# Kernel optimization log

Hardware: AMD Instinct MI355X
Metric: run time of the kernel (lower is better)

The kernel has to match this reference:

```python
import jax, jax.numpy as jnp
import numpy as np

B, S1, S2, D, H, FFN = 4, 1024, 1024, 1024, 16, 4096
DK = D // H  # 64
EPS = 1e-5


def layer_norm(x, g, b):
    m = jnp.mean(x, axis=-1, keepdims=True)
    v = jnp.mean((x - m) ** 2, axis=-1, keepdims=True)
    return (x - m) * jax.lax.rsqrt(v + EPS) * g + b


def cross_attention(y, kvn, mask, qw, kw, vw, ow, ob):
    # y: [B,S1,D], kvn: [B,S2,D], mask: [B,S2] int (0 -> masked)
    q = (y @ qw).reshape(B, S1, H, DK)
    k = (kvn @ kw).reshape(B, S2, H, DK)
    v = (kvn @ vw).reshape(B, S2, H, DK)
    attn = jnp.einsum('bqhd,bkhd->bhqk', q, k) / np.sqrt(DK).astype(np.float32)
    attn = jnp.where(mask[:, None, None, :] == 0, jnp.float32(-1e9), attn)
    attn = jax.nn.softmax(attn, axis=-1)
    out = jnp.einsum('bhqk,bkhd->bqhd', attn, v).reshape(B, S1, H * DK)
    return out @ ow + ob


def setup_inputs() -> dict:
    key = jax.random.key(0)
    ks = jax.random.split(key, 16)
    s = 1.0 / np.sqrt(D)
    inp = {
        'x': jax.random.normal(ks[0], (B, S1, D), jnp.float32),
        'kv': jax.random.normal(ks[1], (B, S2, D), jnp.float32),
        'attn_bias': jax.random.randint(ks[2], (B, S2), 0, 2, jnp.int32),
        'ln1_g': jnp.ones((D,), jnp.float32),
        'ln1_b': jnp.zeros((D,), jnp.float32),
        'qw0': jax.random.normal(ks[3], (D, D), jnp.float32) * s,
        'kw0': jax.random.normal(ks[4], (D, D), jnp.float32) * s,
        'vw0': jax.random.normal(ks[5], (D, D), jnp.float32) * s,
        'ow0': jax.random.normal(ks[6], (D, D), jnp.float32) * s,
        'ob0': jnp.zeros((D,), jnp.float32),
        'qw1': jax.random.normal(ks[7], (D, D), jnp.float32) * s,
        'kw1': jax.random.normal(ks[8], (D, D), jnp.float32) * s,
        'vw1': jax.random.normal(ks[9], (D, D), jnp.float32) * s,
        'ow1': jax.random.normal(ks[10], (D, D), jnp.float32) * s,
        'ob1': jnp.zeros((D,), jnp.float32),
        'ln2_g': jnp.ones((D,), jnp.float32),
        'ln2_b': jnp.zeros((D,), jnp.float32),
        'w1': jax.random.normal(ks[11], (D, FFN), jnp.float32) * s,
        'b1': jnp.zeros((FFN,), jnp.float32),
        'w2': jax.random.normal(ks[12], (FFN, D), jnp.float32) * (1.0 / np.sqrt(FFN)),
        'b2': jnp.zeros((D,), jnp.float32),
    }
    return inp


def reference(x, kv, attn_bias, ln1_g, ln1_b, qw0, kw0, vw0, ow0, ob0,
              qw1, kw1, vw1, ow1, ob1, ln2_g, ln2_b, w1, b1, w2, b2):
    y = layer_norm(x, ln1_g, ln1_b)
    kvn = layer_norm(kv, ln1_g, ln1_b)  # same norm module applied to both
    y = cross_attention(y, kvn, attn_bias, qw0, kw0, vw0, ow0, ob0) + y
    y = cross_attention(y, kvn, attn_bias, qw1, kw1, vw1, ow1, ob1) + y
    x = x + y  # dropout rate 0 -> identity
    y = layer_norm(x, ln2_g, ln2_b)
    y = jax.nn.relu(y @ w1 + b1) @ w2 + b2
    x = x + y
    return x
```

## Files before the change

### kernel.cpp

```cpp
#include <hip/hip_runtime.h>
#include <stdint.h>

typedef unsigned short u16;
typedef __bf16 bf16x8 __attribute__((ext_vector_type(8)));
typedef float f32x4 __attribute__((ext_vector_type(4)));

#define LOG2E 1.4426950408889634f

__device__ __forceinline__ float bf2f(u16 a) {
  union { unsigned u; float f; } v; v.u = ((unsigned)a) << 16; return v.f;
}
__device__ __forceinline__ u16 f2bf(float f) {
  union { float f; unsigned u; } v; v.f = f;
  unsigned r = v.u + 0x7fffu + ((v.u >> 16) & 1u);
  return (u16)(r >> 16);
}
__device__ __forceinline__ u16 f2bf_fast(float f) {
  __bf16 h = (__bf16)f;
  union { __bf16 h; u16 u; } v; v.h = h; return v.u;
}
__device__ __forceinline__ void gl_lds16(const void* g, void* l) {
  __builtin_amdgcn_global_load_lds(
      (const __attribute__((address_space(1))) uint32_t*)g,
      (__attribute__((address_space(3))) uint32_t*)l,
      16, 0, 0);
}

__device__ __forceinline__ int swz(int row, int colu16) {
  return row * 64 + (colu16 ^ (((row ^ (row >> 2)) & 7) << 3));
}

template <int BM, int BN, int MODE>
__global__ __launch_bounds__(256) void gemm_bt(
    const u16* __restrict__ A, const u16* __restrict__ Bt,
    u16* Cbf, float* C32,
    const float* __restrict__ bias,
    const u16* resbf, const float* __restrict__ resx,
    int M, int N, int K, const int* __restrict__ rowcnt)
{
  constexpr int MT = BM / 32, NT = BN / 32;
  constexpr int GA = BM / 32, GB = BN / 32;
  __shared__ u16 sA[BM * 64];
  __shared__ u16 sB[BN * 64];
  const int tid  = threadIdx.x;
  const int wave = tid >> 6, lane = tid & 63;
  const int quad = lane >> 4, l16 = lane & 15;
  const int wm = wave >> 1, wn = wave & 1;
  const int nwg = gridDim.x * gridDim.y;
  const int bid = blockIdx.y * gridDim.x + blockIdx.x;
  const int sw  = (bid & 7) * (nwg >> 3) + (bid >> 3);
  const int m0 = (sw / gridDim.x) * BM, n0 = (sw % gridDim.x) * BN;
  if (rowcnt) {
    int lim = (rowcnt[m0 >> 10] + 63) & ~63;
    if ((m0 & 1023) >= lim) return;
  }

  f32x4 acc[MT][NT] = {};

  for (int k0 = 0; k0 < K; k0 += 64) {
    __syncthreads();
#pragma unroll
    for (int i = 0; i < GA; ++i) {
      int cb = i * 256 + wave * 64;
      int c = cb + lane;
      int row = c >> 3;
      int kcs = (c & 7) ^ ((row ^ (row >> 2)) & 7);
      gl_lds16(A + (size_t)(m0 + row) * K + k0 + kcs * 8, &sA[cb * 8]);
    }
#pragma unroll
    for (int i = 0; i < GB; ++i) {
      int cb = i * 256 + wave * 64;
      int c = cb + lane;
      int row = c >> 3;
      int kcs = (c & 7) ^ ((row ^ (row >> 2)) & 7);
      gl_lds16(Bt + (size_t)(n0 + row) * K + k0 + kcs * 8, &sB[cb * 8]);
    }
    __syncthreads();

#pragma unroll
    for (int kk = 0; kk < 2; ++kk) {
      bf16x8 fa[MT], fb[NT];
#pragma unroll
      for (int mt = 0; mt < MT; ++mt)
        fa[mt] = *(const bf16x8*)&sA[swz(wm * (BM / 2) + mt * 16 + l16, kk * 32 + quad * 8)];
#pragma unroll
      for (int nt = 0; nt < NT; ++nt)
        fb[nt] = *(const bf16x8*)&sB[swz(wn * (BN / 2) + nt * 16 + l16, kk * 32 + quad * 8)];
#pragma unroll
      for (int mt = 0; mt < MT; ++mt)
#pragma unroll
        for (int nt = 0; nt < NT; ++nt)
          acc[mt][nt] = __builtin_amdgcn_mfma_f32_16x16x32_bf16(
              fa[mt], fb[nt], acc[mt][nt], 0, 0, 0);
    }
  }

#pragma unroll
  for (int mt = 0; mt < MT; ++mt) {
#pragma unroll
    for (int nt = 0; nt < NT; ++nt) {
#pragma unroll
      for (int r = 0; r < 4; ++r) {
        int row = m0 + wm * (BM / 2) + mt * 16 + quad * 4 + r;
        int col = n0 + wn * (BN / 2) + nt * 16 + l16;
        size_t idx = (size_t)row * N + col;
        float v = acc[mt][nt][r];
        if constexpr (MODE == 0) {
          Cbf[idx] = f2bf(v);
        } else if constexpr (MODE == 1) {
          v += bias[col] + bf2f(resbf[idx]);
          Cbf[idx] = f2bf(v);
        } else if constexpr (MODE == 2) {
          v = fmaxf(v + bias[col], 0.f);
          Cbf[idx] = f2bf(v);
        } else if constexpr (MODE == 3) {
          v += bias[col] + resx[idx] + bf2f(resbf[idx]);
          C32[idx] = v;
        } else {
          C32[idx] = C32[idx] + v;
        }
      }
    }
  }
}

__global__ __launch_bounds__(256) void transpose64(
    const float* __restrict__ in, u16* __restrict__ out, int R, int Cstride)
{
  __shared__ u16 tile[64][72];
  const int r0 = blockIdx.y * 64, c0 = blockIdx.x * 64;
  const int t = threadIdx.x;
  {
    const int lr = t >> 4, lc = (t & 15) * 4;
#pragma unroll
    for (int h = 0; h < 4; ++h) {
      int row = h * 16 + lr;
      float4 vd = *(const float4*)&in[(size_t)(r0 + row) * Cstride + c0 + lc];
      ushort4 ov;
      ov.x = f2bf(vd.x); ov.y = f2bf(vd.y); ov.z = f2bf(vd.z); ov.w = f2bf(vd.w);
      *(ushort4*)&tile[row][lc] = ov;
    }
  }
  __syncthreads();
  {
    const int lr = t >> 3, lv = t & 7;
#pragma unroll
    for (int h = 0; h < 2; ++h) {
      int orow = h * 32 + lr;
      u16 tmp[8];
#pragma unroll
      for (int j = 0; j < 8; ++j) tmp[j] = tile[lv * 8 + j][orow];
      *(uint4*)&out[(size_t)(c0 + orow) * R + r0 + lv * 8] = *(uint4*)tmp;
    }
  }
}

__global__ __launch_bounds__(256) void mask_scan(
    const int* __restrict__ mask, int* __restrict__ sidx, int* __restrict__ nv)
{
  const int b = blockIdx.x, t = threadIdx.x;
  const int wave = t >> 6, lane = t & 63;
  int m[4]; int cnt = 0;
#pragma unroll
  for (int k = 0; k < 4; ++k) { m[k] = (mask[b * 1024 + t * 4 + k] != 0); cnt += m[k]; }
  int sc = cnt;
  for (int sh = 1; sh < 64; sh <<= 1) {
    int u = __shfl_up(sc, sh);
    if (lane >= sh) sc += u;
  }
  __shared__ int wsum[4];
  if (lane == 63) wsum[wave] = sc;
  __syncthreads();
  int woff = 0;
  for (int w = 0; w < wave; ++w) woff += wsum[w];
  int pos = woff + sc - cnt;
#pragma unroll
  for (int k = 0; k < 4; ++k)
    if (m[k]) sidx[b * 1024 + pos++] = t * 4 + k;
  if (t == 255) nv[b] = wsum[0] + wsum[1] + wsum[2] + wsum[3];
}

__global__ __launch_bounds__(256) void gather_kv(
    const u16* __restrict__ src, const int* __restrict__ sidx,
    const int* __restrict__ nv, u16* __restrict__ dst)
{
  const int t = threadIdx.x, wave = t >> 6, lane = t & 63;
  const int row = blockIdx.x * 4 + wave;
  const int b = row >> 10, i = row & 1023;
  const int n = nv[b];
  const int s = sidx[b * 1024 + (i < n ? i : n - 1)];
  const uint4* sp = (const uint4*)&src[((size_t)(b << 10) + s) * 1024];
  uint4* dp = (uint4*)&dst[(size_t)row * 1024];
  dp[lane] = sp[lane];
  dp[lane + 64] = sp[lane + 64];
}

__global__ __launch_bounds__(256) void vtc_kernel(
    const u16* __restrict__ in, const int* __restrict__ nv,
    u16* __restrict__ out)
{
  __shared__ u16 tile[64][72];
  const int st = blockIdx.x, bh = blockIdx.y;
  const int b = bh >> 4, h = bh & 15;
  const int t = threadIdx.x;
  const int lr = t >> 3, lv = t & 7;
  const int n = nv[b];
  const u16* srcb = in + (size_t)b * 1024 * 2048 + 1024 + h * 64;
#pragma unroll
  for (int half = 0; half < 2; ++half) {
    int i = st * 64 + half * 32 + lr;
    int s = i < n ? i : n - 1;
    uint4 vd = *(const uint4*)&srcb[(size_t)s * 2048 + lv * 8];
    *(uint4*)&tile[half * 32 + lr][lv * 8] = vd;
  }
  __syncthreads();
  u16* dst = out + (size_t)bh * 64 * 1024 + st * 64;
#pragma unroll
  for (int half = 0; half < 2; ++half) {
    int orow = half * 32 + lr;
    u16 tmp[8];
#pragma unroll
    for (int j = 0; j < 8; ++j) tmp[j] = tile[lv * 8 + j][orow];
    *(uint4*)&dst[(size_t)orow * 1024 + lv * 8] = *(uint4*)tmp;
  }
}

__global__ __launch_bounds__(256) void ln_kernel(
    const float* __restrict__ x, const float* __restrict__ g,
    const float* __restrict__ b, u16* __restrict__ outbf)
{
  const int row = blockIdx.x, t = threadIdx.x;
  const int wave = t >> 6, lane = t & 63;
  float4 xv = *(const float4*)&x[(size_t)row * 1024 + t * 4];
  float v0 = xv.x, v1 = xv.y, v2 = xv.z, v3 = xv.w;
  float s = v0 + v1 + v2 + v3;
  float s2 = v0 * v0 + v1 * v1 + v2 * v2 + v3 * v3;
  for (int m = 1; m < 64; m <<= 1) { s += __shfl_xor(s, m); s2 += __shfl_xor(s2, m); }
  __shared__ float ps[4], pq[4];
  if (lane == 0) { ps[wave] = s; pq[wave] = s2; }
  __syncthreads();
  s = ps[0] + ps[1] + ps[2] + ps[3];
  s2 = pq[0] + pq[1] + pq[2] + pq[3];
  float mean = s * (1.f / 1024.f);
  float var = s2 * (1.f / 1024.f) - mean * mean;
  float rs = rsqrtf(var + 1e-5f);
  float4 gv = *(const float4*)&g[t * 4];
  float4 bv = *(const float4*)&b[t * 4];
  ushort4 ov;
  ov.x = f2bf((v0 - mean) * rs * gv.x + bv.x);
  ov.y = f2bf((v1 - mean) * rs * gv.y + bv.y);
  ov.z = f2bf((v2 - mean) * rs * gv.z + bv.z);
  ov.w = f2bf((v3 - mean) * rs * gv.w + bv.w);
  *(ushort4*)&outbf[(size_t)row * 1024 + t * 4] = ov;
}

__global__ __launch_bounds__(256) void ln_add_kernel(
    const float* __restrict__ x, const u16* __restrict__ ybf,
    const float* __restrict__ g, const float* __restrict__ b,
    u16* __restrict__ hbf)
{
  const int row = blockIdx.x, t = threadIdx.x;
  const int wave = t >> 6, lane = t & 63;
  float4 xv = *(const float4*)&x[(size_t)row * 1024 + t * 4];
  ushort4 yv = *(const ushort4*)&ybf[(size_t)row * 1024 + t * 4];
  float v0 = xv.x + bf2f(yv.x), v1 = xv.y + bf2f(yv.y);
  float v2 = xv.z + bf2f(yv.z), v3 = xv.w + bf2f(yv.w);
  float s = v0 + v1 + v2 + v3;
  float s2 = v0 * v0 + v1 * v1 + v2 * v2 + v3 * v3;
  for (int m = 1; m < 64; m <<= 1) { s += __shfl_xor(s, m); s2 += __shfl_xor(s2, m); }
  __shared__ float ps[4], pq[4];
  if (lane == 0) { ps[wave] = s; pq[wave] = s2; }
  __syncthreads();
  s = ps[0] + ps[1] + ps[2] + ps[3];
  s2 = pq[0] + pq[1] + pq[2] + pq[3];
  float mean = s * (1.f / 1024.f);
  float var = s2 * (1.f / 1024.f) - mean * mean;
  float rs = rsqrtf(var + 1e-5f);
  float4 gv = *(const float4*)&g[t * 4];
  float4 bv = *(const float4*)&b[t * 4];
  ushort4 ov;
  ov.x = f2bf((v0 - mean) * rs * gv.x + bv.x);
  ov.y = f2bf((v1 - mean) * rs * gv.y + bv.y);
  ov.z = f2bf((v2 - mean) * rs * gv.z + bv.z);
  ov.w = f2bf((v3 - mean) * rs * gv.w + bv.w);
  *(ushort4*)&hbf[(size_t)row * 1024 + t * 4] = ov;
}

__global__ __launch_bounds__(256) void attn_kernel(
    const u16* __restrict__ Q,
    const u16* __restrict__ K,
    const u16* __restrict__ Vt,
    const int* __restrict__ nvp,
    u16* __restrict__ O)
{
  __shared__ u16 sK[64 * 64], sVt[64 * 64], sP[128 * 64];
  const int h = blockIdx.x, qt = blockIdx.y, b = blockIdx.z;
  const int t = threadIdx.x;
  const int wave = t >> 6, lane = t & 63;
  const int quad = lane >> 4, l16 = lane & 15;
  const u16* Qb = Q + (size_t)b * 1024 * 1024 + (size_t)qt * 128 * 1024 + h * 64;
  const u16* Kb = K + (size_t)b * 1024 * 2048 + h * 64;
  const u16* Vb = Vt + (size_t)(b * 16 + h) * 64 * 1024;
  const int n = nvp[b];
  const int jmax = (n + 63) >> 6;

#pragma unroll
  for (int i = 0; i < 4; ++i) {
    int cb = i * 256 + wave * 64;
    int c = cb + lane;
    int row = c >> 3;
    int scc = (c & 7) ^ ((row ^ (row >> 2)) & 7);
    gl_lds16(Qb + (size_t)row * 1024 + scc * 8, &sP[cb * 8]);
  }
  __syncthreads();
  bf16x8 aq[2][2];
#pragma unroll
  for (int g = 0; g < 2; ++g)
#pragma unroll
    for (int ks = 0; ks < 2; ++ks)
      aq[g][ks] = *(const bf16x8*)&sP[swz(wave * 32 + g * 16 + l16, ks * 32 + quad * 8)];

  float m2_[2][4], l_[2][4];
  f32x4 accO[2][4] = {};
#pragma unroll
  for (int g = 0; g < 2; ++g)
#pragma unroll
    for (int r = 0; r < 4; ++r) { m2_[g][r] = -1e30f; l_[g][r] = 0.f; }

  constexpr float QS = 0.125f * LOG2E;

  for (int j = 0; j < jmax; ++j) {
    __syncthreads();
#pragma unroll
    for (int i = 0; i < 2; ++i) {
      int cb = i * 256 + wave * 64;
      int c = cb + lane;
      int row = c >> 3;
      int scc = (c & 7) ^ ((row ^ (row >> 2)) & 7);
      gl_lds16(Kb + (size_t)(j * 64 + row) * 2048 + scc * 8, &sK[cb * 8]);
      gl_lds16(Vb + (size_t)row * 1024 + j * 64 + scc * 8, &sVt[cb * 8]);
    }
    __syncthreads();

    float mf[4];
#pragma unroll
    for (int nt = 0; nt < 4; ++nt)
      mf[nt] = (j * 64 + nt * 16 + l16 < n) ? 0.f : -1e9f;

#pragma unroll
    for (int g = 0; g < 2; ++g) {
      f32x4 accS[4] = {};
#pragma unroll
      for (int ks = 0; ks < 2; ++ks) {
#pragma unroll
        for (int nt = 0; nt < 4; ++nt) {
          bf16x8 bk = *(const bf16x8*)&sK[swz(nt * 16 + l16, ks * 32 + quad * 8)];
          accS[nt] = __builtin_amdgcn_mfma_f32_16x16x32_bf16(aq[g][ks], bk, accS[nt], 0, 0, 0);
        }
      }
      float vv[4][4], cm_[4];
      bool need = false;
#pragma unroll
      for (int r = 0; r < 4; ++r) {
#pragma unroll
        for (int nt = 0; nt < 4; ++nt) vv[r][nt] = fmaf(accS[nt][r], QS, mf[nt]);
        float cm = fmaxf(fmaxf(vv[r][0], vv[r][1]), fmaxf(vv[r][2], vv[r][3]));
        for (int sh = 1; sh < 16; sh <<= 1) cm = fmaxf(cm, __shfl_xor(cm, sh));
        cm_[r] = cm;
        need = need || (cm > m2_[g][r] + 8.f);
      }
      if (__any(need)) {
#pragma unroll
        for (int r = 0; r < 4; ++r) {
          float nm = fmaxf(m2_[g][r], cm_[r]);
          float al = exp2f(m2_[g][r] - nm);
          m2_[g][r] = nm;
          l_[g][r] *= al;
#pragma unroll
          for (int n2 = 0; n2 < 4; ++n2) accO[g][n2][r] *= al;
        }
      }
#pragma unroll
      for (int r = 0; r < 4; ++r) {
        int prow = wave * 32 + g * 16 + quad * 4 + r;
        float rs = 0.f;
#pragma unroll
        for (int nt = 0; nt < 4; ++nt) {
          float p = exp2f(vv[r][nt] - m2_[g][r]);
          rs += p;
          sP[swz(prow, nt * 16 + l16)] = f2bf_fast(p);
        }
        l_[g][r] += rs;
      }
    }
#pragma unroll
    for (int ks = 0; ks < 2; ++ks) {
      bf16x8 bv[4];
#pragma unroll
      for (int n2 = 0; n2 < 4; ++n2)
        bv[n2] = *(const bf16x8*)&sVt[swz(n2 * 16 + l16, ks * 32 + quad * 8)];
#pragma unroll
      for (int g = 0; g < 2; ++g) {
        bf16x8 ap = *(const bf16x8*)&sP[swz(wave * 32 + g * 16 + l16, ks * 32 + quad * 8)];
#pragma unroll
        for (int n2 = 0; n2 < 4; ++n2)
          accO[g][n2] = __builtin_amdgcn_mfma_f32_16x16x32_bf16(ap, bv[n2], accO[g][n2], 0, 0, 0);
      }
    }
  }

  u16* Ob = O + (size_t)b * 1024 * 1024 + (size_t)qt * 128 * 1024 + h * 64;
#pragma unroll
  for (int g = 0; g < 2; ++g) {
#pragma unroll
    for (int r = 0; r < 4; ++r) {
      float lr = l_[g][r];
      for (int sh = 1; sh < 16; sh <<= 1) lr += __shfl_xor(lr, sh);
      float inv = 1.f / lr;
      int row = wave * 32 + g * 16 + quad * 4 + r;
#pragma unroll
      for (int n2 = 0; n2 < 4; ++n2)
        Ob[(size_t)row * 1024 + n2 * 16 + l16] = f2bf_fast(accO[g][n2][r] * inv);
    }
  }
}

extern "C" void kernel_launch(void* const* d_in, const int* in_sizes, int n_in,
                              void* d_out, int out_size, void* d_ws, size_t ws_size,
                              hipStream_t stream)
{
  const float* x   = (const float*)d_in[0];
  const float* kv  = (const float*)d_in[1];
  const int* attn_bias = (const int*)d_in[2];
  const float* ln1_g = (const float*)d_in[3];
  const float* ln1_b = (const float*)d_in[4];
  const float* qw0 = (const float*)d_in[5];
  const float* kw0 = (const float*)d_in[6];
  const float* vw0 = (const float*)d_in[7];
  const float* ow0 = (const float*)d_in[8];
  const float* ob0 = (const float*)d_in[9];
  const float* qw1 = (const float*)d_in[10];
  const float* kw1 = (const float*)d_in[11];
  const float* vw1 = (const float*)d_in[12];
  const float* ow1 = (const float*)d_in[13];
  const float* ob1 = (const float*)d_in[14];
  const float* ln2_g = (const float*)d_in[15];
  const float* ln2_b = (const float*)d_in[16];
  const float* w1 = (const float*)d_in[17];
  const float* b1 = (const float*)d_in[18];
  const float* w2 = (const float*)d_in[19];
  const float* b2 = (const float*)d_in[20];

  char* ws = (char*)d_ws;
  const size_t MB = 1u << 20;
  u16* Wkv   = (u16*)(ws + 0 * MB);
  u16* Wsm   = (u16*)(ws + 4 * MB);
  int* sidx  = (int*)(ws + 6 * MB);
  int* nvp   = sidx + 4096;
  u16* wtA   = (u16*)(ws + 0 * MB);
  u16* wtB   = (u16*)(ws + 4 * MB);
  u16* ybf   = (u16*)(ws + 8 * MB);
  u16* kvc   = (u16*)(ws + 16 * MB);
  u16* qbuf  = (u16*)(ws + 24 * MB);
  u16* kvbuf = (u16*)(ws + 32 * MB);
  u16* hbf   = kvc;
  u16* fbuf  = kvbuf;
  u16* attnb = (u16*)d_out;
  u16* vT    = (u16*)((char*)d_out + 8 * MB);
  float* out32 = (float*)d_out;

  const dim3 B256(256);
  const dim3 gT(16, 16);
  const dim3 gGemmN1k(8, 64);
  const dim3 gGemm2k(16, 64);
  const dim3 gVt(16, 64);
  const dim3 gAttn(16, 8, 4);

  mask_scan<<<4, B256, 0, stream>>>(attn_bias, sidx, nvp);

  ln_kernel<<<4096, B256, 0, stream>>>(x,  ln1_g, ln1_b, ybf);
  ln_kernel<<<4096, B256, 0, stream>>>(kv, ln1_g, ln1_b, qbuf);
  gather_kv<<<1024, B256, 0, stream>>>(qbuf, sidx, nvp, kvc);

  for (int layer = 0; layer < 2; ++layer) {
    const float* qw = layer ? qw1 : qw0;
    const float* kw = layer ? kw1 : kw0;
    const float* vw = layer ? vw1 : vw0;
    const float* ow = layer ? ow1 : ow0;
    const float* ob = layer ? ob1 : ob0;

    transpose64<<<gT, B256, 0, stream>>>(kw, Wkv, 1024, 1024);
    transpose64<<<gT, B256, 0, stream>>>(vw, Wkv + 1024 * 1024, 1024, 1024);
    gemm_bt<64, 128, 0><<<gGemm2k, B256, 0, stream>>>(
        kvc, Wkv, kvbuf, nullptr, nullptr, nullptr, nullptr,
        4096, 2048, 1024, nvp);
    transpose64<<<gT, B256, 0, stream>>>(qw, Wsm, 1024, 1024);
    gemm_bt<64, 128, 0><<<gGemmN1k, B256, 0, stream>>>(
        ybf, Wsm, qbuf, nullptr, nullptr, nullptr, nullptr,
        4096, 1024, 1024, nullptr);
    vtc_kernel<<<gVt, B256, 0, stream>>>(kvbuf, nvp, vT);

    attn_kernel<<<gAttn, B256, 0, stream>>>(qbuf, kvbuf, vT, nvp, attnb);

    transpose64<<<gT, B256, 0, stream>>>(ow, Wsm, 1024, 1024);
    gemm_bt<64, 128, 1><<<gGemmN1k, B256, 0, stream>>>(
        attnb, Wsm, ybf, nullptr, ob, ybf, nullptr,
        4096, 1024, 1024, nullptr);
  }

  ln_add_kernel<<<4096, B256, 0, stream>>>(x, ybf, ln2_g, ln2_b, hbf);

  for (int band = 0; band < 2; ++band) {
    transpose64<<<dim3(32, 16), B256, 0, stream>>>(w1 + band * 2048, wtA, 1024, 4096);
    transpose64<<<dim3(16, 32), B256, 0, stream>>>(w2 + (size_t)band * 2048 * 1024,
                                                   wtB, 2048, 1024);
    gemm_bt<64, 128, 2><<<gGemm2k, B256, 0, stream>>>(
        hbf, wtA, fbuf, nullptr, b1 + band * 2048, nullptr, nullptr,
        4096, 2048, 1024, nullptr);
    if (band == 0) {
      gemm_bt<64, 128, 3><<<gGemmN1k, B256, 0, stream>>>(
          fbuf, wtB, nullptr, out32, b2, ybf, x, 4096, 1024, 2048, nullptr);
    } else {
      gemm_bt<64, 128, 4><<<gGemmN1k, B256, 0, stream>>>(
          fbuf, wtB, nullptr, out32, nullptr, nullptr, nullptr,
          4096, 1024, 2048, nullptr);
    }
  }
}
```

Before: 534.2 us.

## Double attention key block size to 128 per iteration

The attention kernel now processes 128 keys per loop iteration instead of 64. It stages larger K, V^T and P tiles in LDS with a 128-wide swizzle for V^T and P, which halves the number of barriers and online-softmax rescale checks per row. The K/V GEMM row-count cutoff is rounded to 128 so that the padded rows the wider tile reads are computed. In exchange the kernel uses more LDS (64KB) and registers, which may lower occupancy, and more padded keys may be processed.

New measurement: 564.2 us. 5.6% more time.

```diff
diff --git a/kernel.cpp b/kernel.cpp
--- a/kernel.cpp
+++ b/kernel.cpp
@@ -26,8 +26,12 @@
       16, 0, 0);
 }
 
+__device__ __forceinline__ int swzf(int row) { return (row ^ (row >> 2)) & 7; }
 __device__ __forceinline__ int swz(int row, int colu16) {
-  return row * 64 + (colu16 ^ (((row ^ (row >> 2)) & 7) << 3));
+  return row * 64 + (colu16 ^ (swzf(row) << 3));
+}
+__device__ __forceinline__ int swz128(int row, int colu16) {
+  return row * 128 + (colu16 ^ (swzf(row) << 3));
 }
 
 template <int BM, int BN, int MODE>
@@ -51,7 +55,7 @@
   const int sw  = (bid & 7) * (nwg >> 3) + (bid >> 3);
   const int m0 = (sw / gridDim.x) * BM, n0 = (sw % gridDim.x) * BN;
   if (rowcnt) {
-    int lim = (rowcnt[m0 >> 10] + 63) & ~63;
+    int lim = (rowcnt[m0 >> 10] + 127) & ~127;
     if ((m0 & 1023) >= lim) return;
   }
 
@@ -64,7 +68,7 @@
       int cb = i * 256 + wave * 64;
       int c = cb + lane;
       int row = c >> 3;
-      int kcs = (c & 7) ^ ((row ^ (row >> 2)) & 7);
+      int kcs = (c & 7) ^ swzf(row);
       gl_lds16(A + (size_t)(m0 + row) * K + k0 + kcs * 8, &sA[cb * 8]);
     }
 #pragma unroll
@@ -72,7 +76,7 @@
       int cb = i * 256 + wave * 64;
       int c = cb + lane;
       int row = c >> 3;
-      int kcs = (c & 7) ^ ((row ^ (row >> 2)) & 7);
+      int kcs = (c & 7) ^ swzf(row);
       gl_lds16(Bt + (size_t)(n0 + row) * K + k0 + kcs * 8, &sB[cb * 8]);
     }
     __syncthreads();
@@ -293,7 +297,7 @@
     const int* __restrict__ nvp,
     u16* __restrict__ O)
 {
-  __shared__ u16 sK[64 * 64], sVt[64 * 64], sP[128 * 64];
+  __shared__ u16 sK[128 * 64], sVt[64 * 128], sP[128 * 128];
   const int h = blockIdx.x, qt = blockIdx.y, b = blockIdx.z;
   const int t = threadIdx.x;
   const int wave = t >> 6, lane = t & 63;
@@ -302,14 +306,14 @@
   const u16* Kb = K + (size_t)b * 1024 * 2048 + h * 64;
   const u16* Vb = Vt + (size_t)(b * 16 + h) * 64 * 1024;
   const int n = nvp[b];
-  const int jmax = (n + 63) >> 6;
+  const int jmax = (n + 127) >> 7;
 
 #pragma unroll
   for (int i = 0; i < 4; ++i) {
     int cb = i * 256 + wave * 64;
     int c = cb + lane;
     int row = c >> 3;
-    int scc = (c & 7) ^ ((row ^ (row >> 2)) & 7);
+    int scc = (c & 7) ^ swzf(row);
     gl_lds16(Qb + (size_t)row * 1024 + scc * 8, &sP[cb * 8]);
   }
   __syncthreads();
@@ -332,39 +336,49 @@
   for (int j = 0; j < jmax; ++j) {
     __syncthreads();
 #pragma unroll
-    for (int i = 0; i < 2; ++i) {
+    for (int i = 0; i < 4; ++i) {
       int cb = i * 256 + wave * 64;
       int c = cb + lane;
       int row = c >> 3;
-      int scc = (c & 7) ^ ((row ^ (row >> 2)) & 7);
-      gl_lds16(Kb + (size_t)(j * 64 + row) * 2048 + scc * 8, &sK[cb * 8]);
-      gl_lds16(Vb + (size_t)row * 1024 + j * 64 + scc * 8, &sVt[cb * 8]);
+      int scc = (c & 7) ^ swzf(row);
+      gl_lds16(Kb + (size_t)(j * 128 + row) * 2048 + scc * 8, &sK[cb * 8]);
+    }
+#pragma unroll
+    for (int i = 0; i < 4; ++i) {
+      int cb = i * 256 + wave * 64;
+      int c = cb + lane;
+      int row = c >> 4;
+      int scc = (c & 15) ^ swzf(row);
+      gl_lds16(Vb + (size_t)row * 1024 + j * 128 + scc * 8, &sVt[cb * 8]);
     }
     __syncthreads();
 
-    float mf[4];
-#pragma unroll
-    for (int nt = 0; nt < 4; ++nt)
-      mf[nt] = (j * 64 + nt * 16 + l16 < n) ? 0.f : -1e9f;
+    float mf[8];
+#pragma unroll
+    for (int nt = 0; nt < 8; ++nt)
+      mf[nt] = (j * 128 + nt * 16 + l16 < n) ? 0.f : -1e9f;
 
 #pragma unroll
     for (int g = 0; g < 2; ++g) {
-      f32x4 accS[4] = {};
+      f32x4 accS[8] = {};
 #pragma unroll
       for (int ks = 0; ks < 2; ++ks) {
 #pragma unroll
-        for (int nt = 0; nt < 4; ++nt) {
+        for (int nt = 0; nt < 8; ++nt) {
           bf16x8 bk = *(const bf16x8*)&sK[swz(nt * 16 + l16, ks * 32 + quad * 8)];
           accS[nt] = __builtin_amdgcn_mfma_f32_16x16x32_bf16(aq[g][ks], bk, accS[nt], 0, 0, 0);
         }
       }
-      float vv[4][4], cm_[4];
+      float vv[4][8], cm_[4];
       bool need = false;
 #pragma unroll
       for (int r = 0; r < 4; ++r) {
-#pragma unroll
-        for (int nt = 0; nt < 4; ++nt) vv[r][nt] = fmaf(accS[nt][r], QS, mf[nt]);
-        float cm = fmaxf(fmaxf(vv[r][0], vv[r][1]), fmaxf(vv[r][2], vv[r][3]));
+        float cm = -1e30f;
+#pragma unroll
+        for (int nt = 0; nt < 8; ++nt) {
+          vv[r][nt] = fmaf(accS[nt][r], QS, mf[nt]);
+          cm = fmaxf(cm, vv[r][nt]);
+        }
         for (int sh = 1; sh < 16; sh <<= 1) cm = fmaxf(cm, __shfl_xor(cm, sh));
         cm_[r] = cm;
         need = need || (cm > m2_[g][r] + 8.f);
@@ -385,23 +399,23 @@
         int prow = wave * 32 + g * 16 + quad * 4 + r;
         float rs = 0.f;
 #pragma unroll
-        for (int nt = 0; nt < 4; ++nt) {
+        for (int nt = 0; nt < 8; ++nt) {
           float p = exp2f(vv[r][nt] - m2_[g][r]);
           rs += p;
-          sP[swz(prow, nt * 16 + l16)] = f2bf_fast(p);
+          sP[swz128(prow, nt * 16 + l16)] = f2bf_fast(p);
         }
         l_[g][r] += rs;
       }
     }
 #pragma unroll
-    for (int ks = 0; ks < 2; ++ks) {
+    for (int ks = 0; ks < 4; ++ks) {
       bf16x8 bv[4];
 #pragma unroll
       for (int n2 = 0; n2 < 4; ++n2)
-        bv[n2] = *(const bf16x8*)&sVt[swz(n2 * 16 + l16, ks * 32 + quad * 8)];
+        bv[n2] = *(const bf16x8*)&sVt[swz128(n2 * 16 + l16, ks * 32 + quad * 8)];
 #pragma unroll
       for (int g = 0; g < 2; ++g) {
-        bf16x8 ap = *(const bf16x8*)&sP[swz(wave * 32 + g * 16 + l16, ks * 32 + quad * 8)];
+        bf16x8 ap = *(const bf16x8*)&sP[swz128(wave * 32 + g * 16 + l16, ks * 32 + quad * 8)];
 #pragma unroll
         for (int n2 = 0; n2 < 4; ++n2)
           accO[g][n2] = __builtin_amdgcn_mfma_f32_16x16x32_bf16(ap, bv[n2], accO[g][n2], 0, 0, 0);
```
